# Optimization experiments

Measured on AMD Instinct MI355X. Metric: run time of the kernel, lower is better.

Reference implementation:

```python
import jax, jax.numpy as jnp
import numpy as np
import math

B, L, D, H, DEPTH = 2, 1024, 1024, 16, 4
INNER = int(D * 4 * 2 / 3)  # 2730
HD = D // H
SCALE = D ** 0.5


def _get_slopes(n):
    def pow2(n):
        start = 2 ** (-2 ** (-(math.log2(n) - 3)))
        return [start * start ** i for i in range(n)]
    if math.log2(n).is_integer():
        return pow2(n)
    c = 2 ** math.floor(math.log2(n))
    return pow2(c) + _get_slopes(2 * c)[0::2][: n - c]


def setup_inputs() -> dict:
    key = jax.random.key(0)
    ks = jax.random.split(key, 8)
    def rn(k, shape, s=0.02):
        return jax.random.normal(k, shape, dtype=jnp.float32) * s
    return {
        "x": jax.random.normal(ks[0], (B, L, D), dtype=jnp.float32),
        "slopes": jnp.asarray(np.asarray(_get_slopes(H), dtype=np.float32).reshape(H, 1, 1)),
        "gamma_attn": jnp.ones((DEPTH, D), jnp.float32),
        "in_proj_w": rn(ks[1], (DEPTH, 3 * D, D)),
        "in_proj_b": jnp.zeros((DEPTH, 3 * D), jnp.float32),
        "out_proj_w": rn(ks[2], (DEPTH, D, D)),
        "out_proj_b": jnp.zeros((DEPTH, D), jnp.float32),
        "gamma_ff": jnp.ones((DEPTH, D), jnp.float32),
        "ff_w1": rn(ks[3], (DEPTH, 2 * INNER, D)),
        "ff_b1": jnp.zeros((DEPTH, 2 * INNER), jnp.float32),
        "ff_w2": rn(ks[4], (DEPTH, D, INNER)),
        "ff_b2": jnp.zeros((DEPTH, D), jnp.float32),
        "final_gamma": jnp.ones((D,), jnp.float32),
    }


def _rmsnorm(t, gamma):
    # F.normalize(x, dim=-1) * sqrt(dim) * gamma
    n = jnp.linalg.norm(t, axis=-1, keepdims=True)
    return t / jnp.maximum(n, 1e-12) * SCALE * gamma


def reference(x, slopes, gamma_attn, in_proj_w, in_proj_b, out_proj_w, out_proj_b,
              gamma_ff, ff_w1, ff_b1, ff_w2, ff_b2, final_gamma):
    Bsz, Ls, Dm = x.shape
    pos = jnp.arange(Ls)
    # ALiBi bias: -(|i-j|) * per-head slope -> (H, L, L); shared across batch
    alibi = (-jnp.abs(pos[None, :] - pos[:, None]).astype(jnp.float32))[None] * slopes
    for i in range(DEPTH):
        # attention block
        a_in = _rmsnorm(x, gamma_attn[i])
        qkv = a_in @ in_proj_w[i].T + in_proj_b[i]  # (B, L, 3D)
        q, k, v = jnp.split(qkv, 3, axis=-1)
        q = q.reshape(Bsz, Ls, H, HD).transpose(0, 2, 1, 3)
        k = k.reshape(Bsz, Ls, H, HD).transpose(0, 2, 1, 3)
        v = v.reshape(Bsz, Ls, H, HD).transpose(0, 2, 1, 3)
        scores = jnp.einsum('bhqd,bhkd->bhqk', q, k) / math.sqrt(HD) + alibi[None]
        attn = jax.nn.softmax(scores, axis=-1)
        o = jnp.einsum('bhqk,bhkd->bhqd', attn, v).transpose(0, 2, 1, 3).reshape(Bsz, Ls, Dm)
        x = o @ out_proj_w[i].T + out_proj_b[i] + x
        # GEGLU feed-forward block
        f_in = _rmsnorm(x, gamma_ff[i])
        h = f_in @ ff_w1[i].T + ff_b1[i]
        a, gate = jnp.split(h, 2, axis=-1)
        x = (jax.nn.gelu(gate, approximate=False) * a) @ ff_w2[i].T + ff_b2[i] + x
    return _rmsnorm(x, final_gamma)
```

## Files before the change

### kernel.cpp

```cpp
#include <hip/hip_runtime.h>

#define DEPTH   4
#define BSZ     2
#define LSEQ    1024
#define DMODEL  1024
#define NHEAD   16
#define HDIM    64
#define MROWS   (BSZ*LSEQ)
#define INNER   2730
#define INNERP  2752
#define N1      (2*INNER)
#define N1P     (2*INNERP)
#define LOG2E   1.4426950408889634f
#define NSPLIT  2

typedef __bf16 bf16;
typedef bf16  bf16x8 __attribute__((ext_vector_type(8)));
typedef float f32x4  __attribute__((ext_vector_type(4)));
typedef uint32_t u32x4 __attribute__((ext_vector_type(4)));

__device__ inline f32x4 mfma16(bf16x8 a, bf16x8 b, f32x4 c) {
  return __builtin_amdgcn_mfma_f32_16x16x32_bf16(a, b, c, 0, 0, 0);
}

__device__ inline void gload_lds16(const void* g, void* l) {
  __builtin_amdgcn_global_load_lds(
      (const __attribute__((address_space(1))) void*)g,
      (__attribute__((address_space(3))) void*)l, 16, 0, 0);
}

__global__ void conv_bf16_kernel(const float* __restrict__ src, bf16* __restrict__ dst, size_t n) {
  size_t i = ((size_t)blockIdx.x * 256 + threadIdx.x) * 8;
  if (i >= n) return;
  float4 v0 = *(const float4*)(src + i);
  float4 v1 = *(const float4*)(src + i + 4);
  bf16x8 o = { (bf16)v0.x,(bf16)v0.y,(bf16)v0.z,(bf16)v0.w,
               (bf16)v1.x,(bf16)v1.y,(bf16)v1.z,(bf16)v1.w };
  *(bf16x8*)(dst + i) = o;
}

__global__ void conv_w1_kernel(const float* __restrict__ src, bf16* __restrict__ dst) {
  size_t i = ((size_t)blockIdx.x * 256 + threadIdx.x) * 8;
  const size_t tot = (size_t)DEPTH * N1P * DMODEL;
  if (i >= tot) return;
  int d  = (int)(i / ((size_t)N1P * DMODEL));
  int rem = (int)(i % ((size_t)N1P * DMODEL));
  int rp = rem / DMODEL, k = rem % DMODEL;
  int p2 = rp >> 4, w = rp & 15;
  int col = ((p2 >> 1) << 4) + w;
  bf16x8 o;
  if (col >= INNER) {
    o = (bf16x8)(bf16)0.f;
  } else {
    int rs = (p2 & 1) ? (INNER + col) : col;
    const float* s = src + ((size_t)d * N1 + rs) * DMODEL + k;
    float4 v0 = *(const float4*)s;
    float4 v1 = *(const float4*)(s + 4);
    o = bf16x8{ (bf16)v0.x,(bf16)v0.y,(bf16)v0.z,(bf16)v0.w,
                (bf16)v1.x,(bf16)v1.y,(bf16)v1.z,(bf16)v1.w };
  }
  *(bf16x8*)(dst + i) = o;
}

__global__ void conv_b1_kernel(const float* __restrict__ src, float* __restrict__ dst) {
  int i = blockIdx.x * 256 + threadIdx.x;
  if (i >= DEPTH * N1P) return;
  int d = i / N1P, rp = i % N1P;
  int p2 = rp >> 4, w = rp & 15;
  int col = ((p2 >> 1) << 4) + w;
  float v = 0.f;
  if (col < INNER) v = src[d * N1 + ((p2 & 1) ? (INNER + col) : col)];
  dst[i] = v;
}

__global__ void conv_w2_kernel(const float* __restrict__ src, bf16* __restrict__ dst) {
  size_t i = ((size_t)blockIdx.x * 256 + threadIdx.x) * 8;
  const size_t tot = (size_t)DEPTH * DMODEL * INNERP;
  if (i >= tot) return;
  size_t dn = i / INNERP;
  int kp = (int)(i % INNERP);
  const float* s = src + dn * INNER;
  bf16x8 o;
  #pragma unroll
  for (int j = 0; j < 8; ++j) {
    int k = kp + j;
    o[j] = (k < INNER) ? (bf16)s[k] : (bf16)0.f;
  }
  *(bf16x8*)(dst + i) = o;
}

template<bool OUT_BF16>
__global__ __launch_bounds__(256) void rmsnorm_kernel(const float* __restrict__ x,
    const float* __restrict__ gamma, void* __restrict__ out) {
  const int row = blockIdx.x;
  const int tid = threadIdx.x;
  const float4 v = *(const float4*)(x + (size_t)row * DMODEL + tid * 4);
  float ss = v.x*v.x + v.y*v.y + v.z*v.z + v.w*v.w;
  for (int m = 1; m < 64; m <<= 1) ss += __shfl_xor(ss, m);
  __shared__ float ws4[4];
  if ((tid & 63) == 0) ws4[tid >> 6] = ss;
  __syncthreads();
  float tot = ws4[0] + ws4[1] + ws4[2] + ws4[3];
  float scale = 32.0f / fmaxf(sqrtf(tot), 1e-12f);
  const float4 g = *(const float4*)(gamma + tid * 4);
  float o0 = v.x*scale*g.x, o1 = v.y*scale*g.y, o2 = v.z*scale*g.z, o3 = v.w*scale*g.w;
  size_t p = (size_t)row * DMODEL + tid * 4;
  if (OUT_BF16) {
    bf16* ob = (bf16*)out;
    ob[p+0] = (bf16)o0; ob[p+1] = (bf16)o1; ob[p+2] = (bf16)o2; ob[p+3] = (bf16)o3;
  } else {
    *(float4*)((float*)out + p) = make_float4(o0, o1, o2, o3);
  }
}

template<int TN, int EPI, bool CHUNK_M>
__global__ __launch_bounds__(256) void gemm_bt(const bf16* __restrict__ A,
    const bf16* __restrict__ Bw, const float* __restrict__ bias,
    void* __restrict__ Cout, int M_, int N_, int Kstr, int nk0, int nkTot) {
  constexpr int NFR = TN / 32;
  constexpr int BCH = TN / 32;
  __shared__ __attribute__((aligned(16))) bf16 As[2][128 * 64];
  __shared__ __attribute__((aligned(16))) bf16 Bs[2][TN * 64];
  const int tid  = threadIdx.x;
  const int lane = tid & 63;
  const int wid  = tid >> 6;
  const int wr = wid >> 1, wc = wid & 1;

  const int z = blockIdx.z;
  const int nk  = z ? (nkTot - nk0) : nk0;
  const int kOff = z * (nk0 << 6);

  const int gx = gridDim.x, gy = gridDim.y;
  const int nwg = gx * gy;
  int bid = blockIdx.y * gx + blockIdx.x;
  int swz = bid;
  if ((nwg & 7) == 0) swz = (bid & 7) * (nwg >> 3) + (bid >> 3);
  int mIdx, nIdx;
  if (CHUNK_M) { nIdx = swz % gx; mIdx = swz / gx; }
  else         { mIdx = swz % gy; nIdx = swz / gy; }
  const int m0 = mIdx * 128;
  const int n0 = nIdx * TN;

  const int q = lane & 15, G = lane >> 4;
  const int s7 = q & 7;
  const int srow = tid >> 3;
  const int scol = ((tid & 7) ^ (srow & 7)) << 3;

  f32x4 acc[4][NFR] = {};

  auto stage = [&](int buf, int kt) {
    const int k0 = kOff + (kt << 6);
    #pragma unroll
    for (int j = 0; j < 4; ++j) {
      gload_lds16(A + (size_t)(m0 + j*32 + srow) * Kstr + k0 + scol,
                  &As[buf][(j * 256 + wid * 64) << 3]);
    }
    #pragma unroll
    for (int j = 0; j < BCH; ++j) {
      gload_lds16(Bw + (size_t)(n0 + j*32 + srow) * Kstr + k0 + scol,
                  &Bs[buf][(j * 256 + wid * 64) << 3]);
    }
  };

  stage(0, 0);
  if (nk > 1) stage(1, 1);

  int cur = 0;
  for (int kt = 0; kt < nk; ++kt) {
    if (kt < nk - 1) {
      if constexpr (TN == 64) asm volatile("s_waitcnt vmcnt(6)" ::: "memory");
      else                    asm volatile("s_waitcnt vmcnt(8)" ::: "memory");
    } else {
      asm volatile("s_waitcnt vmcnt(0)" ::: "memory");
    }
    __builtin_amdgcn_s_barrier();
    asm volatile("" ::: "memory");

    #pragma unroll
    for (int kk = 0; kk < 2; ++kk) {
      const int c0 = kk * 4 + G;
      bf16x8 af[4], bfr[NFR];
      #pragma unroll
      for (int m = 0; m < 4; ++m)
        af[m] = *(const bf16x8*)(&As[cur][(wr*64 + m*16 + q) * 64 + ((c0 ^ s7) << 3)]);
      #pragma unroll
      for (int n = 0; n < NFR; ++n)
        bfr[n] = *(const bf16x8*)(&Bs[cur][(wc*(TN/2) + n*16 + q) * 64 + ((c0 ^ s7) << 3)]);
      #pragma unroll
      for (int m = 0; m < 4; ++m)
        #pragma unroll
        for (int n = 0; n < NFR; ++n)
          acc[m][n] = mfma16(af[m], bfr[n], acc[m][n]);
    }

    asm volatile("s_waitcnt lgkmcnt(0)" ::: "memory");
    __builtin_amdgcn_s_barrier();
    asm volatile("" ::: "memory");
    if (kt + 2 < nk) stage(cur, kt + 2);
    cur ^= 1;
  }

  const int rb = G << 2;
  const int cl = q;
  if (EPI == 2) {
    #pragma unroll
    for (int m = 0; m < 4; ++m) {
      #pragma unroll
      for (int np = 0; np < NFR/2; ++np) {
        int ca = n0 + wc*(TN/2) + (2*np)*16 + cl;
        int cg = ca + 16;
        float ba = bias[ca], bg = bias[cg];
        int colo = ((ca >> 5) << 4) + cl;
        #pragma unroll
        for (int r = 0; r < 4; ++r) {
          int row = m0 + wr*64 + m*16 + rb + r;
          float av = acc[m][2*np][r] + ba;
          float gv = acc[m][2*np+1][r] + bg;
          float gl = 0.5f * gv * (1.f + erff(gv * 0.70710678118654752f));
          ((bf16*)Cout)[(size_t)row * (N_ >> 1) + colo] = (bf16)(av * gl);
        }
      }
    }
  } else if (EPI == 3) {
    #pragma unroll
    for (int m = 0; m < 4; ++m) {
      #pragma unroll
      for (int n = 0; n < NFR; ++n) {
        int col = n0 + wc*(TN/2) + n*16 + cl;
        float bv = (z == 0) ? bias[col] : 0.f;
        #pragma unroll
        for (int r = 0; r < 4; ++r) {
          int row = m0 + wr*64 + m*16 + rb + r;
          atomicAdd((float*)Cout + (size_t)row * N_ + col, acc[m][n][r] + bv);
        }
      }
    }
  } else {
    #pragma unroll
    for (int m = 0; m < 4; ++m) {
      #pragma unroll
      for (int n = 0; n < NFR; ++n) {
        int col = n0 + wc*(TN/2) + n*16 + cl;
        float bv = bias[col];
        #pragma unroll
        for (int r = 0; r < 4; ++r) {
          int row = m0 + wr*64 + m*16 + rb + r;
          ((bf16*)Cout)[(size_t)row * N_ + col] = (bf16)(acc[m][n][r] + bv);
        }
      }
    }
  }
}

__global__ __launch_bounds__(256) void attn_kernel(const bf16* __restrict__ qkv,
    const float* __restrict__ slopes, float* __restrict__ Opart, float* __restrict__ ml) {
  const int tid = threadIdx.x, lane = tid & 63, wid = tid >> 6;
  const int bh = blockIdx.y;
  const int b = bh >> 4, h = bh & 15;
  const int kvz = blockIdx.z;
  const int kv0 = kvz * (LSEQ / NSPLIT);
  const float slope2 = slopes[h] * LOG2E;
  const float SC = 0.125f * LOG2E;
  const int qw = blockIdx.x * 64 + wid * 16;

  __shared__ __attribute__((aligned(16))) bf16     Kt[64 * 72];
  __shared__ __attribute__((aligned(16))) uint32_t V32[64 * 36];

  const size_t rs = 3 * DMODEL;
  const size_t base = (size_t)b * LSEQ * rs;
  const int q = lane & 15, G = lane >> 4;
  const float qi = (float)(qw + q);

  bf16x8 qf[2];
  {
    const bf16* p = qkv + base + (size_t)(qw + q) * rs + h * HDIM + (G << 3);
    qf[0] = *(const bf16x8*)p;
    qf[1] = *(const bf16x8*)(p + 32);
  }

  f32x4 accO[4] = {};
  float mreg = -1e30f, lreg = 0.f;

  const int trow = tid >> 2;
  const int tcol = (tid & 3) << 4;

  bf16x8 kreg0, kreg1, vreg0, vreg1;
  {
    const bf16* kp = qkv + base + (size_t)(kv0 + trow) * rs + DMODEL + h * HDIM + tcol;
    kreg0 = *(const bf16x8*)kp; kreg1 = *(const bf16x8*)(kp + 8);
    const bf16* vp = qkv + base + (size_t)(kv0 + trow) * rs + 2 * DMODEL + h * HDIM + tcol;
    vreg0 = *(const bf16x8*)vp; vreg1 = *(const bf16x8*)(vp + 8);
  }

  for (int kv = kv0; kv < kv0 + LSEQ / NSPLIT; kv += 64) {
    __syncthreads();
    *(bf16x8*)(Kt + trow * 72 + tcol)     = kreg0;
    *(bf16x8*)(Kt + trow * 72 + tcol + 8) = kreg1;
    {
      u32x4 va = __builtin_bit_cast(u32x4, vreg0);
      u32x4 vb = __builtin_bit_cast(u32x4, vreg1);
      u32x4 pa, pb;
      #pragma unroll
      for (int i = 0; i < 4; ++i) {
        pa[i] = (uint32_t)__shfl_xor((int)va[i], 4);
        pb[i] = (uint32_t)__shfl_xor((int)vb[i], 4);
      }
      const bool oddk = (trow & 1);
      const int d0 = tcol + (oddk ? 8 : 0);
      u32x4 m = oddk ? vb : va;
      u32x4 oo = oddk ? pb : pa;
      const int kpair = trow >> 1;
      const int swz = kpair ^ ((d0 >> 3) << 1);
      #pragma unroll
      for (int i = 0; i < 4; ++i) {
        uint32_t lo = oddk ? oo[i] : m[i];
        uint32_t hi = oddk ? m[i] : oo[i];
        uint32_t w0 = (lo & 0xffffu) | (hi << 16);
        uint32_t w1 = (lo >> 16) | (hi & 0xffff0000u);
        V32[(d0 + 2*i)     * 36 + swz] = w0;
        V32[(d0 + 2*i + 1) * 36 + swz] = w1;
      }
    }
    __syncthreads();

    if (kv + 64 < kv0 + LSEQ / NSPLIT) {
      const bf16* kp = qkv + base + (size_t)(kv + 64 + trow) * rs + DMODEL + h * HDIM + tcol;
      kreg0 = *(const bf16x8*)kp; kreg1 = *(const bf16x8*)(kp + 8);
      const bf16* vp = qkv + base + (size_t)(kv + 64 + trow) * rs + 2 * DMODEL + h * HDIM + tcol;
      vreg0 = *(const bf16x8*)vp; vreg1 = *(const bf16x8*)(vp + 8);
    }

    f32x4 sacc[4] = {};
    __builtin_amdgcn_s_setprio(1);
    #pragma unroll
    for (int nt = 0; nt < 4; ++nt) {
      const bf16* kb = Kt + (nt * 16 + q) * 72 + (G << 3);
      sacc[nt] = mfma16(*(const bf16x8*)kb, qf[0], sacc[nt]);
      sacc[nt] = mfma16(*(const bf16x8*)(kb + 32), qf[1], sacc[nt]);
    }
    __builtin_amdgcn_s_setprio(0);

    float pv[4][4];
    float pmax = -1e30f;
    #pragma unroll
    for (int nt = 0; nt < 4; ++nt) {
      #pragma unroll
      for (int r = 0; r < 4; ++r) {
        float kj = (float)(kv + nt * 16 + (G << 2) + r);
        float s = sacc[nt][r] * SC - slope2 * fabsf(qi - kj);
        pv[nt][r] = s;
        pmax = fmaxf(pmax, s);
      }
    }
    pmax = fmaxf(pmax, __shfl_xor(pmax, 16));
    pmax = fmaxf(pmax, __shfl_xor(pmax, 32));

    if (!__all(pmax <= mreg + 8.f)) {
      float mnew = fmaxf(mreg, pmax);
      float ef = exp2f(mreg - mnew);
      mreg = mnew;
      lreg *= ef;
      float efr[4];
      #pragma unroll
      for (int r = 0; r < 4; ++r)
        efr[r] = __shfl(ef, (G << 4) + (G << 2) + r);
      #pragma unroll
      for (int dn = 0; dn < 4; ++dn)
        #pragma unroll
        for (int r = 0; r < 4; ++r)
          accO[dn][r] *= efr[r];
    }

    float rsum = 0.f;
    #pragma unroll
    for (int nt = 0; nt < 4; ++nt) {
      #pragma unroll
      for (int r = 0; r < 4; ++r) {
        float pe = exp2f(pv[nt][r] - mreg);
        pv[nt][r] = pe;
        rsum += pe;
      }
    }
    rsum += __shfl_xor(rsum, 16);
    rsum += __shfl_xor(rsum, 32);
    lreg += rsum;

    uint32_t wp[4][2];
    #pragma unroll
    for (int nt = 0; nt < 4; ++nt) {
      asm("v_cvt_pk_bf16_f32 %0, %1, %2" : "=v"(wp[nt][0]) : "v"(pv[nt][0]), "v"(pv[nt][1]));
      asm("v_cvt_pk_bf16_f32 %0, %1, %2" : "=v"(wp[nt][1]) : "v"(pv[nt][2]), "v"(pv[nt][3]));
    }

    __builtin_amdgcn_s_setprio(1);
    #pragma unroll
    for (int chunk = 0; chunk < 2; ++chunk) {
      u32x4 u;
      #pragma unroll
      for (int j = 0; j < 4; ++j) {
        int src = (((G & 1) * 2 + (j >> 1)) << 4) | q;
        uint32_t lo2 = (uint32_t)__shfl((int)wp[2*chunk][j & 1], src);
        uint32_t hi2 = (uint32_t)__shfl((int)wp[2*chunk + 1][j & 1], src);
        u[j] = (G & 2) ? hi2 : lo2;
      }
      bf16x8 pf = __builtin_bit_cast(bf16x8, u);
      #pragma unroll
      for (int dn = 0; dn < 4; ++dn) {
        const int d = dn * 16 + q;
        u32x4 raw = *(const u32x4*)(V32 + d * 36 + chunk * 16 + 4 * (G ^ dn));
        if ((lane >> 3) & 1) raw = __builtin_shufflevector(raw, raw, 2, 3, 0, 1);
        bf16x8 vf = __builtin_bit_cast(bf16x8, raw);
        accO[dn] = mfma16(pf, vf, accO[dn]);
      }
    }
    __builtin_amdgcn_s_setprio(0);
  }

  #pragma unroll
  for (int r = 0; r < 4; ++r) {
    int qr = qw + (G << 2) + r;
    size_t obase = ((size_t)(kvz * 32 + bh) * LSEQ + qr) * HDIM;
    #pragma unroll
    for (int dn = 0; dn < 4; ++dn)
      Opart[obase + dn * 16 + q] = accO[dn][r];
  }
  if (lane < 16) {
    size_t mb = ((size_t)(kvz * 32 + bh) * LSEQ + qw + lane) * 2;
    ml[mb]     = mreg;
    ml[mb + 1] = lreg;
  }
}

__global__ __launch_bounds__(256) void attn_combine(const float* __restrict__ Opart,
    const float* __restrict__ ml, bf16* __restrict__ o) {
  int idx = blockIdx.x * 256 + threadIdx.x;
  int bh = idx >> 14;
  int rem = idx & 16383;
  int qr = rem >> 4;
  int d4 = (rem & 15) << 2;
  float mz[NSPLIT], lz[NSPLIT];
  float m = -1e30f;
  #pragma unroll
  for (int z = 0; z < NSPLIT; ++z) {
    size_t rz = ((size_t)(z * 32 + bh) * LSEQ + qr) * 2;
    mz[z] = ml[rz]; lz[z] = ml[rz + 1];
    m = fmaxf(m, mz[z]);
  }
  float wz[NSPLIT];
  float l = 0.f;
  #pragma unroll
  for (int z = 0; z < NSPLIT; ++z) { wz[z] = exp2f(mz[z] - m); l += lz[z] * wz[z]; }
  float inv = 1.f / l;
  float ax = 0, ay = 0, az = 0, aw = 0;
  #pragma unroll
  for (int z = 0; z < NSPLIT; ++z) {
    size_t rz = (size_t)(z * 32 + bh) * LSEQ + qr;
    float4 ov = *(const float4*)(Opart + rz * HDIM + d4);
    ax += ov.x * wz[z]; ay += ov.y * wz[z]; az += ov.z * wz[z]; aw += ov.w * wz[z];
  }
  int b = bh >> 4, h = bh & 15;
  bf16* op = o + ((size_t)(b * LSEQ + qr) * DMODEL + h * HDIM + d4);
  op[0] = (bf16)(ax * inv);
  op[1] = (bf16)(ay * inv);
  op[2] = (bf16)(az * inv);
  op[3] = (bf16)(aw * inv);
}

extern "C" void kernel_launch(void* const* d_in, const int* in_sizes, int n_in,
                              void* d_out, int out_size, void* d_ws, size_t ws_size,
                              hipStream_t stream) {
  const float* x_in      = (const float*)d_in[0];
  const float* slopes    = (const float*)d_in[1];
  const float* g_attn    = (const float*)d_in[2];
  const float* w_in      = (const float*)d_in[3];
  const float* b_in      = (const float*)d_in[4];
  const float* w_out     = (const float*)d_in[5];
  const float* b_out     = (const float*)d_in[6];
  const float* g_ff      = (const float*)d_in[7];
  const float* w1        = (const float*)d_in[8];
  const float* b1        = (const float*)d_in[9];
  const float* w2        = (const float*)d_in[10];
  const float* b2        = (const float*)d_in[11];
  const float* g_final   = (const float*)d_in[12];

  char* p = (char*)d_ws;
  float* xw   = (float*)p;              p += (size_t)MROWS * DMODEL * 4;
  bf16* abuf  = (bf16*)p;               p += (size_t)MROWS * DMODEL * 2;
  bf16* qkvb  = (bf16*)p;               p += (size_t)MROWS * 3 * DMODEL * 2;
  bf16* obuf  = (bf16*)p;               p += (size_t)MROWS * DMODEL * 2;
  bf16* gbuf  = (bf16*)p;               p += (size_t)MROWS * INNERP * 2;
  float* Opart = (float*)p;             p += (size_t)NSPLIT * 32 * LSEQ * HDIM * 4;
  float* mlb   = (float*)p;             p += (size_t)NSPLIT * 32 * LSEQ * 2 * 4;
  bf16* w_in_b  = (bf16*)p;             p += (size_t)DEPTH * 3 * DMODEL * DMODEL * 2;
  bf16* w_out_b = (bf16*)p;             p += (size_t)DEPTH * DMODEL * DMODEL * 2;
  bf16* w1p     = (bf16*)p;             p += (size_t)DEPTH * N1P * DMODEL * 2;
  bf16* w2p     = (bf16*)p;             p += (size_t)DEPTH * DMODEL * INNERP * 2;
  float* b1p    = (float*)p;            p += (size_t)DEPTH * N1P * 4;

  hipMemcpyAsync(xw, x_in, (size_t)MROWS * DMODEL * 4, hipMemcpyDeviceToDevice, stream);

  conv_bf16_kernel<<<6144, 256, 0, stream>>>(w_in, w_in_b, (size_t)DEPTH * 3 * DMODEL * DMODEL);
  conv_bf16_kernel<<<2048, 256, 0, stream>>>(w_out, w_out_b, (size_t)DEPTH * DMODEL * DMODEL);
  conv_w1_kernel<<<11008, 256, 0, stream>>>(w1, w1p);
  conv_b1_kernel<<<86, 256, 0, stream>>>(b1, b1p);
  conv_w2_kernel<<<5504, 256, 0, stream>>>(w2, w2p);

  for (int i = 0; i < DEPTH; ++i) {
    rmsnorm_kernel<true><<<MROWS, 256, 0, stream>>>(xw, g_attn + i * DMODEL, abuf);
    gemm_bt<64, 0, false><<<dim3(48, 16), 256, 0, stream>>>(
        abuf, w_in_b + (size_t)i * 3 * DMODEL * DMODEL, b_in + i * 3 * DMODEL,
        qkvb, MROWS, 3 * DMODEL, DMODEL, 16, 16);
    attn_kernel<<<dim3(16, 32, NSPLIT), 256, 0, stream>>>(qkvb, slopes, Opart, mlb);
    attn_combine<<<2048, 256, 0, stream>>>(Opart, mlb, obuf);
    gemm_bt<64, 3, true><<<dim3(16, 16, 2), 256, 0, stream>>>(
        obuf, w_out_b + (size_t)i * DMODEL * DMODEL, b_out + i * DMODEL,
        xw, MROWS, DMODEL, DMODEL, 8, 16);
    rmsnorm_kernel<true><<<MROWS, 256, 0, stream>>>(xw, g_ff + i * DMODEL, abuf);
    gemm_bt<64, 2, false><<<dim3(86, 16), 256, 0, stream>>>(
        abuf, w1p + (size_t)i * N1P * DMODEL, b1p + i * N1P,
        gbuf, MROWS, N1P, DMODEL, 16, 16);
    gemm_bt<64, 3, true><<<dim3(16, 16, 2), 256, 0, stream>>>(
        gbuf, w2p + (size_t)i * DMODEL * INNERP, b2 + i * DMODEL,
        xw, MROWS, DMODEL, INNERP, 22, 43);
  }
  rmsnorm_kernel<false><<<MROWS, 256, 0, stream>>>(xw, g_final, d_out);
}
```

Baseline: 699.0 us.

## Process 128-key tiles per attention iteration and split-K GEMMs three ways

The attention kernel now stages two 64-row K/V tiles (128 keys) per iteration in larger shared buffers and processes them as two halves, so it needs half as many barriers and prefetch rounds. The split-K GEMM gains a generalized chunk count, and the out-projection and FF2 GEMMs are launched with three K-splits instead of two, which adds more blocks to raise occupancy. The cost is doubled LDS and more registers in attention, plus more atomic or accumulation traffic into the residual from the extra split.

New measurement: 737.8 us. +5.5%, slower.

```diff
diff --git a/kernel.cpp b/kernel.cpp
--- a/kernel.cpp
+++ b/kernel.cpp
@@ -127,7 +127,8 @@
   const int wr = wid >> 1, wc = wid & 1;
 
   const int z = blockIdx.z;
-  const int nk  = z ? (nkTot - nk0) : nk0;
+  const int rem = nkTot - z * nk0;
+  const int nk  = rem < nk0 ? rem : nk0;
   const int kOff = z * (nk0 << 6);
 
   const int gx = gridDim.x, gy = gridDim.y;
@@ -263,8 +264,8 @@
   const float SC = 0.125f * LOG2E;
   const int qw = blockIdx.x * 64 + wid * 16;
 
-  __shared__ __attribute__((aligned(16))) bf16     Kt[64 * 72];
-  __shared__ __attribute__((aligned(16))) uint32_t V32[64 * 36];
+  __shared__ __attribute__((aligned(16))) bf16     Kt[128 * 72];
+  __shared__ __attribute__((aligned(16))) uint32_t V32[64 * 72];
 
   const size_t rs = 3 * DMODEL;
   const size_t base = (size_t)b * LSEQ * rs;
@@ -284,21 +285,28 @@
   const int trow = tid >> 2;
   const int tcol = (tid & 3) << 4;
 
-  bf16x8 kreg0, kreg1, vreg0, vreg1;
+  bf16x8 kA0, kA1, vA0, vA1, kB0, kB1, vB0, vB1;
   {
     const bf16* kp = qkv + base + (size_t)(kv0 + trow) * rs + DMODEL + h * HDIM + tcol;
-    kreg0 = *(const bf16x8*)kp; kreg1 = *(const bf16x8*)(kp + 8);
+    kA0 = *(const bf16x8*)kp; kA1 = *(const bf16x8*)(kp + 8);
     const bf16* vp = qkv + base + (size_t)(kv0 + trow) * rs + 2 * DMODEL + h * HDIM + tcol;
-    vreg0 = *(const bf16x8*)vp; vreg1 = *(const bf16x8*)(vp + 8);
-  }
-
-  for (int kv = kv0; kv < kv0 + LSEQ / NSPLIT; kv += 64) {
+    vA0 = *(const bf16x8*)vp; vA1 = *(const bf16x8*)(vp + 8);
+    const bf16* kp2 = kp + 64 * rs;
+    kB0 = *(const bf16x8*)kp2; kB1 = *(const bf16x8*)(kp2 + 8);
+    const bf16* vp2 = vp + 64 * rs;
+    vB0 = *(const bf16x8*)vp2; vB1 = *(const bf16x8*)(vp2 + 8);
+  }
+
+  for (int kv = kv0; kv < kv0 + LSEQ / NSPLIT; kv += 128) {
     __syncthreads();
-    *(bf16x8*)(Kt + trow * 72 + tcol)     = kreg0;
-    *(bf16x8*)(Kt + trow * 72 + tcol + 8) = kreg1;
-    {
-      u32x4 va = __builtin_bit_cast(u32x4, vreg0);
-      u32x4 vb = __builtin_bit_cast(u32x4, vreg1);
+    #pragma unroll
+    for (int g2 = 0; g2 < 2; ++g2) {
+      bf16x8 k0 = g2 ? kB0 : kA0, k1 = g2 ? kB1 : kA1;
+      bf16x8 v0 = g2 ? vB0 : vA0, v1 = g2 ? vB1 : vA1;
+      *(bf16x8*)(Kt + (g2 * 64 + trow) * 72 + tcol)     = k0;
+      *(bf16x8*)(Kt + (g2 * 64 + trow) * 72 + tcol + 8) = k1;
+      u32x4 va = __builtin_bit_cast(u32x4, v0);
+      u32x4 vb = __builtin_bit_cast(u32x4, v1);
       u32x4 pa, pb;
       #pragma unroll
       for (int i = 0; i < 4; ++i) {
@@ -317,103 +325,111 @@
         uint32_t hi = oddk ? m[i] : oo[i];
         uint32_t w0 = (lo & 0xffffu) | (hi << 16);
         uint32_t w1 = (lo >> 16) | (hi & 0xffff0000u);
-        V32[(d0 + 2*i)     * 36 + swz] = w0;
-        V32[(d0 + 2*i + 1) * 36 + swz] = w1;
+        V32[(d0 + 2*i)     * 72 + g2 * 32 + swz] = w0;
+        V32[(d0 + 2*i + 1) * 72 + g2 * 32 + swz] = w1;
       }
     }
     __syncthreads();
 
-    if (kv + 64 < kv0 + LSEQ / NSPLIT) {
-      const bf16* kp = qkv + base + (size_t)(kv + 64 + trow) * rs + DMODEL + h * HDIM + tcol;
-      kreg0 = *(const bf16x8*)kp; kreg1 = *(const bf16x8*)(kp + 8);
-      const bf16* vp = qkv + base + (size_t)(kv + 64 + trow) * rs + 2 * DMODEL + h * HDIM + tcol;
-      vreg0 = *(const bf16x8*)vp; vreg1 = *(const bf16x8*)(vp + 8);
-    }
-
-    f32x4 sacc[4] = {};
-    __builtin_amdgcn_s_setprio(1);
-    #pragma unroll
-    for (int nt = 0; nt < 4; ++nt) {
-      const bf16* kb = Kt + (nt * 16 + q) * 72 + (G << 3);
-      sacc[nt] = mfma16(*(const bf16x8*)kb, qf[0], sacc[nt]);
-      sacc[nt] = mfma16(*(const bf16x8*)(kb + 32), qf[1], sacc[nt]);
-    }
-    __builtin_amdgcn_s_setprio(0);
-
-    float pv[4][4];
-    float pmax = -1e30f;
-    #pragma unroll
-    for (int nt = 0; nt < 4; ++nt) {
-      #pragma unroll
-      for (int r = 0; r < 4; ++r) {
-        float kj = (float)(kv + nt * 16 + (G << 2) + r);
-        float s = sacc[nt][r] * SC - slope2 * fabsf(qi - kj);
-        pv[nt][r] = s;
-        pmax = fmaxf(pmax, s);
-      }
-    }
-    pmax = fmaxf(pmax, __shfl_xor(pmax, 16));
-    pmax = fmaxf(pmax, __shfl_xor(pmax, 32));
-
-    if (!__all(pmax <= mreg + 8.f)) {
-      float mnew = fmaxf(mreg, pmax);
-      float ef = exp2f(mreg - mnew);
-      mreg = mnew;
-      lreg *= ef;
-      float efr[4];
-      #pragma unroll
-      for (int r = 0; r < 4; ++r)
-        efr[r] = __shfl(ef, (G << 4) + (G << 2) + r);
-      #pragma unroll
-      for (int dn = 0; dn < 4; ++dn)
+    if (kv + 128 < kv0 + LSEQ / NSPLIT) {
+      const bf16* kp = qkv + base + (size_t)(kv + 128 + trow) * rs + DMODEL + h * HDIM + tcol;
+      kA0 = *(const bf16x8*)kp; kA1 = *(const bf16x8*)(kp + 8);
+      const bf16* vp = qkv + base + (size_t)(kv + 128 + trow) * rs + 2 * DMODEL + h * HDIM + tcol;
+      vA0 = *(const bf16x8*)vp; vA1 = *(const bf16x8*)(vp + 8);
+      const bf16* kp2 = kp + 64 * rs;
+      kB0 = *(const bf16x8*)kp2; kB1 = *(const bf16x8*)(kp2 + 8);
+      const bf16* vp2 = vp + 64 * rs;
+      vB0 = *(const bf16x8*)vp2; vB1 = *(const bf16x8*)(vp2 + 8);
+    }
+
+    #pragma unroll
+    for (int half = 0; half < 2; ++half) {
+      const int kvh = kv + half * 64;
+      f32x4 sacc[4] = {};
+      __builtin_amdgcn_s_setprio(1);
+      #pragma unroll
+      for (int nt = 0; nt < 4; ++nt) {
+        const bf16* kb = Kt + (half * 64 + nt * 16 + q) * 72 + (G << 3);
+        sacc[nt] = mfma16(*(const bf16x8*)kb, qf[0], sacc[nt]);
+        sacc[nt] = mfma16(*(const bf16x8*)(kb + 32), qf[1], sacc[nt]);
+      }
+      __builtin_amdgcn_s_setprio(0);
+
+      float pv[4][4];
+      float pmax = -1e30f;
+      #pragma unroll
+      for (int nt = 0; nt < 4; ++nt) {
+        #pragma unroll
+        for (int r = 0; r < 4; ++r) {
+          float kj = (float)(kvh + nt * 16 + (G << 2) + r);
+          float s = sacc[nt][r] * SC - slope2 * fabsf(qi - kj);
+          pv[nt][r] = s;
+          pmax = fmaxf(pmax, s);
+        }
+      }
+      pmax = fmaxf(pmax, __shfl_xor(pmax, 16));
+      pmax = fmaxf(pmax, __shfl_xor(pmax, 32));
+
+      if (!__all(pmax <= mreg + 8.f)) {
+        float mnew = fmaxf(mreg, pmax);
+        float ef = exp2f(mreg - mnew);
+        mreg = mnew;
+        lreg *= ef;
+        float efr[4];
         #pragma unroll
         for (int r = 0; r < 4; ++r)
-          accO[dn][r] *= efr[r];
-    }
-
-    float rsum = 0.f;
-    #pragma unroll
-    for (int nt = 0; nt < 4; ++nt) {
-      #pragma unroll
-      for (int r = 0; r < 4; ++r) {
-        float pe = exp2f(pv[nt][r] - mreg);
-        pv[nt][r] = pe;
-        rsum += pe;
-      }
-    }
-    rsum += __shfl_xor(rsum, 16);
-    rsum += __shfl_xor(rsum, 32);
-    lreg += rsum;
-
-    uint32_t wp[4][2];
-    #pragma unroll
-    for (int nt = 0; nt < 4; ++nt) {
-      asm("v_cvt_pk_bf16_f32 %0, %1, %2" : "=v"(wp[nt][0]) : "v"(pv[nt][0]), "v"(pv[nt][1]));
-      asm("v_cvt_pk_bf16_f32 %0, %1, %2" : "=v"(wp[nt][1]) : "v"(pv[nt][2]), "v"(pv[nt][3]));
-    }
-
-    __builtin_amdgcn_s_setprio(1);
-    #pragma unroll
-    for (int chunk = 0; chunk < 2; ++chunk) {
-      u32x4 u;
-      #pragma unroll
-      for (int j = 0; j < 4; ++j) {
-        int src = (((G & 1) * 2 + (j >> 1)) << 4) | q;
-        uint32_t lo2 = (uint32_t)__shfl((int)wp[2*chunk][j & 1], src);
-        uint32_t hi2 = (uint32_t)__shfl((int)wp[2*chunk + 1][j & 1], src);
-        u[j] = (G & 2) ? hi2 : lo2;
-      }
-      bf16x8 pf = __builtin_bit_cast(bf16x8, u);
-      #pragma unroll
-      for (int dn = 0; dn < 4; ++dn) {
-        const int d = dn * 16 + q;
-        u32x4 raw = *(const u32x4*)(V32 + d * 36 + chunk * 16 + 4 * (G ^ dn));
-        if ((lane >> 3) & 1) raw = __builtin_shufflevector(raw, raw, 2, 3, 0, 1);
-        bf16x8 vf = __builtin_bit_cast(bf16x8, raw);
-        accO[dn] = mfma16(pf, vf, accO[dn]);
-      }
-    }
-    __builtin_amdgcn_s_setprio(0);
+          efr[r] = __shfl(ef, (G << 4) + (G << 2) + r);
+        #pragma unroll
+        for (int dn = 0; dn < 4; ++dn)
+          #pragma unroll
+          for (int r = 0; r < 4; ++r)
+            accO[dn][r] *= efr[r];
+      }
+
+      float rsum = 0.f;
+      #pragma unroll
+      for (int nt = 0; nt < 4; ++nt) {
+        #pragma unroll
+        for (int r = 0; r < 4; ++r) {
+          float pe = exp2f(pv[nt][r] - mreg);
+          pv[nt][r] = pe;
+          rsum += pe;
+        }
+      }
+      rsum += __shfl_xor(rsum, 16);
+      rsum += __shfl_xor(rsum, 32);
+      lreg += rsum;
+
+      uint32_t wp[4][2];
+      #pragma unroll
+      for (int nt = 0; nt < 4; ++nt) {
+        asm("v_cvt_pk_bf16_f32 %0, %1, %2" : "=v"(wp[nt][0]) : "v"(pv[nt][0]), "v"(pv[nt][1]));
+        asm("v_cvt_pk_bf16_f32 %0, %1, %2" : "=v"(wp[nt][1]) : "v"(pv[nt][2]), "v"(pv[nt][3]));
+      }
+
+      __builtin_amdgcn_s_setprio(1);
+      #pragma unroll
+      for (int chunk = 0; chunk < 2; ++chunk) {
+        u32x4 u;
+        #pragma unroll
+        for (int j = 0; j < 4; ++j) {
+          int src = (((G & 1) * 2 + (j >> 1)) << 4) | q;
+          uint32_t lo2 = (uint32_t)__shfl((int)wp[2*chunk][j & 1], src);
+          uint32_t hi2 = (uint32_t)__shfl((int)wp[2*chunk + 1][j & 1], src);
+          u[j] = (G & 2) ? hi2 : lo2;
+        }
+        bf16x8 pf = __builtin_bit_cast(bf16x8, u);
+        #pragma unroll
+        for (int dn = 0; dn < 4; ++dn) {
+          const int d = dn * 16 + q;
+          u32x4 raw = *(const u32x4*)(V32 + d * 72 + half * 32 + chunk * 16 + 4 * (G ^ dn));
+          if ((lane >> 3) & 1) raw = __builtin_shufflevector(raw, raw, 2, 3, 0, 1);
+          bf16x8 vf = __builtin_bit_cast(bf16x8, raw);
+          accO[dn] = mfma16(pf, vf, accO[dn]);
+        }
+      }
+      __builtin_amdgcn_s_setprio(0);
+    }
   }
 
   #pragma unroll
@@ -512,16 +528,16 @@
         qkvb, MROWS, 3 * DMODEL, DMODEL, 16, 16);
     attn_kernel<<<dim3(16, 32, NSPLIT), 256, 0, stream>>>(qkvb, slopes, Opart, mlb);
     attn_combine<<<2048, 256, 0, stream>>>(Opart, mlb, obuf);
-    gemm_bt<64, 3, true><<<dim3(16, 16, 2), 256, 0, stream>>>(
+    gemm_bt<64, 3, true><<<dim3(16, 16, 3), 256, 0, stream>>>(
         obuf, w_out_b + (size_t)i * DMODEL * DMODEL, b_out + i * DMODEL,
-        xw, MROWS, DMODEL, DMODEL, 8, 16);
+        xw, MROWS, DMODEL, DMODEL, 6, 16);
     rmsnorm_kernel<true><<<MROWS, 256, 0, stream>>>(xw, g_ff + i * DMODEL, abuf);
     gemm_bt<64, 2, false><<<dim3(86, 16), 256, 0, stream>>>(
         abuf, w1p + (size_t)i * N1P * DMODEL, b1p + i * N1P,
         gbuf, MROWS, N1P, DMODEL, 16, 16);
-    gemm_bt<64, 3, true><<<dim3(16, 16, 2), 256, 0, stream>>>(
+    gemm_bt<64, 3, true><<<dim3(16, 16, 3), 256, 0, stream>>>(
         gbuf, w2p + (size_t)i * DMODEL * INNERP, b2 + i * DMODEL,
-        xw, MROWS, DMODEL, INNERP, 22, 43);
+        xw, MROWS, DMODEL, INNERP, 15, 43);
   }
   rmsnorm_kernel<false><<<MROWS, 256, 0, stream>>>(xw, g_final, d_out);
 }
```
